# Optimization experiments

Hardware: AMD Instinct MI355X
Metric: run time of the kernel (lower is better)

Reference implementation:

```python
import jax, jax.numpy as jnp
import numpy as np

VOCAB, EMB, HID = 32000, 512, 512
BATCH, SEQ = 32, 512


def setup_inputs() -> dict:
    key = jax.random.key(0)
    ks = jax.random.split(key, 6)
    return {
        "enc_input": jax.random.randint(ks[0], (BATCH, SEQ), 0, VOCAB),
        "emb": jax.random.normal(ks[1], (VOCAB, EMB), dtype=jnp.float32) * 0.02,
        "W_ih": jax.random.normal(ks[2], (2, 3 * HID, EMB), dtype=jnp.float32) * 0.05,
        "W_hh": jax.random.normal(ks[3], (2, 3 * HID, HID), dtype=jnp.float32) * 0.05,
        "b_ih": jax.random.normal(ks[4], (2, 3 * HID), dtype=jnp.float32) * 0.05,
        "b_hh": jax.random.normal(ks[5], (2, 3 * HID), dtype=jnp.float32) * 0.05,
    }


def _gru_dir(gx, W_hh_d, b_hh_d, H):
    # gx: [B, S, 3H] precomputed input gates; scan left-to-right over S.
    B = gx.shape[0]

    def step(h, gxt):
        gh = h @ W_hh_d.T + b_hh_d  # [B, 3H]
        r = jax.nn.sigmoid(gxt[:, :H] + gh[:, :H])
        z = jax.nn.sigmoid(gxt[:, H:2 * H] + gh[:, H:2 * H])
        n = jnp.tanh(gxt[:, 2 * H:] + r * gh[:, 2 * H:])
        h_new = (1.0 - z) * n + z * h
        return h_new, h_new

    h0 = jnp.zeros((B, H), dtype=gx.dtype)
    hT, ys = jax.lax.scan(step, h0, jnp.swapaxes(gx, 0, 1))  # ys: [S, B, H]
    return jnp.swapaxes(ys, 0, 1), hT


def reference(enc_input, emb, W_ih, W_hh, b_ih, b_hh):
    # NOTE: original torch code feeds the bidirectional GRU one timestep at a
    # time, so BOTH directions effectively run left-to-right over the sequence
    # (each with its own weights). We reproduce that exact behavior.
    H = W_hh.shape[-1]
    x = emb[enc_input]  # [B, S, E]
    # Precompute input-gate projections for both directions in one einsum.
    gx = jnp.einsum('bse,dge->bsdg', x, W_ih) + b_ih  # [B, S, 2, 3H]
    out0, h0 = _gru_dir(gx[:, :, 0, :], W_hh[0], b_hh[0], H)
    out1, h1 = _gru_dir(gx[:, :, 1, :], W_hh[1], b_hh[1], H)
    encoded = jnp.concatenate([out0, out1], axis=-1)  # [B, S, 2H]
    hidden = jnp.stack([h0, h1], axis=0)  # [2, B, H]
    return encoded, hidden
```

## Files before the change

kernel.cpp:

```cpp
#include <hip/hip_runtime.h>
#include <stdint.h>

#define VOCAB 32000
#define EMBD 512
#define HID 512
#define BATCH 32
#define SEQL 512

typedef short bf16x8 __attribute__((ext_vector_type(8)));
typedef short bf16x4 __attribute__((ext_vector_type(4)));
typedef float f32x4 __attribute__((ext_vector_type(4)));

static __device__ __forceinline__ float bf2f(short u) {
  union { unsigned u; float f; } c;
  c.u = ((unsigned)(unsigned short)u) << 16;
  return c.f;
}
static __device__ __forceinline__ unsigned short f2bf(float f) {
  union { float f; unsigned u; } c;
  c.f = f;
  unsigned x = c.u;
  unsigned r = (x + 0x7fffu + ((x >> 16) & 1u)) >> 16;
  return (unsigned short)r;
}

__global__ __launch_bounds__(256) void cvt_f32_bf16(
    const float* __restrict__ src, unsigned short* __restrict__ dst, int n8) {
  int i = blockIdx.x * 256 + threadIdx.x;
  if (i >= n8) return;
  const float4* s = (const float4*)src + (size_t)i * 2;
  float4 a = s[0], b = s[1];
  uint4 p;
  p.x = (unsigned)f2bf(a.x) | ((unsigned)f2bf(a.y) << 16);
  p.y = (unsigned)f2bf(a.z) | ((unsigned)f2bf(a.w) << 16);
  p.z = (unsigned)f2bf(b.x) | ((unsigned)f2bf(b.y) << 16);
  p.w = (unsigned)f2bf(b.z) | ((unsigned)f2bf(b.w) << 16);
  ((uint4*)dst)[i] = p;
}

#define GBM 128
#define GBN 128
#define GBK 64

__global__ __launch_bounds__(256) void gemm_gx(
    const int* __restrict__ enc,
    const unsigned short* __restrict__ embb,
    const unsigned short* __restrict__ wih,
    const float* __restrict__ b_ih,
    unsigned short* __restrict__ gx)
{
  __shared__ __align__(16) unsigned short As[GBM * GBK];
  __shared__ __align__(16) unsigned short Bs[GBN * GBK];
  __shared__ int tokl[GBM];

  const int n0 = blockIdx.x * GBN;
  const int m0 = blockIdx.y * GBM;
  const int tid = threadIdx.x;
  if (tid < GBM) {
    int m = m0 + tid;
    tokl[tid] = enc[(m & 31) * SEQL + (m >> 5)];
  }
  __syncthreads();

  const int l = tid & 63, w = tid >> 6;
  const int wr = w >> 1, wc = w & 1;

  f32x4 acc[4][4];
  f32x4 zero = {0.f, 0.f, 0.f, 0.f};
#pragma unroll
  for (int mt = 0; mt < 4; ++mt)
#pragma unroll
    for (int nt = 0; nt < 4; ++nt) acc[mt][nt] = zero;

  for (int kt = 0; kt < 512; kt += GBK) {
#pragma unroll
    for (int it = 0; it < 4; ++it) {
      int c = it * 256 + tid;
      int r = c >> 3, kc = c & 7;
      uint4 v = *(const uint4*)(embb + (size_t)tokl[r] * 512 + kt + kc * 8);
      unsigned off = (unsigned)(r * 128 + kc * 16); off ^= (r & 7) << 4;
      *(uint4*)((char*)As + off) = v;
    }
#pragma unroll
    for (int it = 0; it < 4; ++it) {
      int c = it * 256 + tid;
      int r = c >> 3, kc = c & 7;
      uint4 v = *(const uint4*)(wih + (size_t)(n0 + r) * 512 + kt + kc * 8);
      unsigned off = (unsigned)(r * 128 + kc * 16); off ^= (r & 7) << 4;
      *(uint4*)((char*)Bs + off) = v;
    }
    __syncthreads();
#pragma unroll
    for (int ks = 0; ks < 2; ++ks) {
      bf16x8 af[4], bfr[4];
#pragma unroll
      for (int mt = 0; mt < 4; ++mt) {
        int r = wr * 64 + mt * 16 + (l & 15);
        unsigned off = (unsigned)(r * 128 + ks * 64 + (l >> 4) * 16);
        off ^= (r & 7) << 4;
        af[mt] = *(const bf16x8*)((char*)As + off);
      }
#pragma unroll
      for (int nt = 0; nt < 4; ++nt) {
        int r = wc * 64 + nt * 16 + (l & 15);
        unsigned off = (unsigned)(r * 128 + ks * 64 + (l >> 4) * 16);
        off ^= (r & 7) << 4;
        bfr[nt] = *(const bf16x8*)((char*)Bs + off);
      }
#pragma unroll
      for (int mt = 0; mt < 4; ++mt)
#pragma unroll
        for (int nt = 0; nt < 4; ++nt)
          acc[mt][nt] = __builtin_amdgcn_mfma_f32_16x16x32_bf16(
              af[mt], bfr[nt], acc[mt][nt], 0, 0, 0);
    }
    __syncthreads();
  }

#pragma unroll
  for (int nt = 0; nt < 4; ++nt) {
    int n = n0 + wc * 64 + nt * 16 + (l & 15);
    int d = n >= 1536 ? 1 : 0;
    int g = n - d * 1536;
    float bias = b_ih[n];
#pragma unroll
    for (int mt = 0; mt < 4; ++mt) {
      int mbase = m0 + wr * 64 + mt * 16 + (l >> 4) * 4;
      int s = mbase >> 5;
      int b = mbase & 31;
      unsigned v0 = (unsigned)f2bf(acc[mt][nt][0] + bias) |
                    ((unsigned)f2bf(acc[mt][nt][1] + bias) << 16);
      unsigned v1 = (unsigned)f2bf(acc[mt][nt][2] + bias) |
                    ((unsigned)f2bf(acc[mt][nt][3] + bias) << 16);
      size_t off = ((size_t)(s * 2 + d) * 1536 + g) * 32 + b;
      uint2 pv; pv.x = v0; pv.y = v1;
      *(uint2*)(gx + off) = pv;
    }
  }
}

#define JW 16
#define NWGD 32

__global__ __launch_bounds__(128) void scan_gru(
    const unsigned short* __restrict__ gx,
    const unsigned short* __restrict__ whh,
    const float* __restrict__ bhh,
    unsigned short* __restrict__ hbuf,
    float* __restrict__ out,
    unsigned* __restrict__ flags)
{
  __shared__ __align__(16) unsigned short Wl[48 * 512];

  const int bid = blockIdx.x;
  const int d = bid >> 5;
  const int wg = bid & 31;
  const int j0 = wg * JW;
  const int tid = threadIdx.x;
  const int l = tid & 63;
  const int w = tid >> 6;

  for (int it = 0; it < 24; ++it) {
    int c = it * 128 + tid;
    int lr = c >> 6, kc = c & 63;
    int gate = lr >> 4, jj = lr & 15;
    uint4 v = *(const uint4*)(whh +
        (size_t)(d * 1536 + gate * 512 + j0 + jj) * 512 + kc * 8);
    unsigned off = (unsigned)(lr * 1024 + kc * 16); off ^= (lr & 7) << 4;
    *(uint4*)((char*)Wl + off) = v;
  }

  const int jl = l & 15;
  const int jglob = j0 + jl;
  const int b0 = w * 16;
  const int brow = b0 + (l >> 4) * 4;
  const float bh_r = bhh[d * 1536 + jglob];
  const float bh_z = bhh[d * 1536 + 512 + jglob];
  const float bh_n = bhh[d * 1536 + 1024 + jglob];

  float hold[4] = {0.f, 0.f, 0.f, 0.f};
  unsigned* myflag = flags + (size_t)(d * 32 + wg) * 16;
  const unsigned* fbase = flags + (size_t)d * 32 * 16;

  __syncthreads();

  bf16x4 gr, gz, gn;
  {
    size_t gb = (size_t)d * 1536 * 32;
    gr = *(const bf16x4*)(gx + gb + (size_t)jglob * 32 + brow);
    gz = *(const bf16x4*)(gx + gb + (size_t)(512 + jglob) * 32 + brow);
    gn = *(const bf16x4*)(gx + gb + (size_t)(1024 + jglob) * 32 + brow);
  }

  for (int t = 0; t < SEQL; ++t) {
    f32x4 accr = {0.f, 0.f, 0.f, 0.f};
    f32x4 accz = accr, accn = accr;

    if (t > 0) {
      const unsigned long long* hq = (const unsigned long long*)
          (hbuf + (size_t)(d * 2 + ((t - 1) & 1)) * 32 * 512);
      size_t qb = (size_t)(b0 + (l & 15)) * 128 + (l >> 4) * 2;
      union { unsigned long long q[2]; bf16x8 v; } afu[16];
#pragma unroll
      for (int ks = 0; ks < 16; ++ks) {
        afu[ks].q[0] = __hip_atomic_load(hq + qb + ks * 8,
                                         __ATOMIC_RELAXED, __HIP_MEMORY_SCOPE_AGENT);
        afu[ks].q[1] = __hip_atomic_load(hq + qb + ks * 8 + 1,
                                         __ATOMIC_RELAXED, __HIP_MEMORY_SCOPE_AGENT);
      }
#pragma unroll
      for (int ks = 0; ks < 16; ++ks) {
        unsigned kb = (unsigned)(ks * 64 + (l >> 4) * 16);
        unsigned r0 = (unsigned)jl, r1 = (unsigned)(16 + jl), r2 = (unsigned)(32 + jl);
        bf16x8 bR = *(const bf16x8*)((char*)Wl + ((r0 * 1024 + kb) ^ ((r0 & 7) << 4)));
        bf16x8 bZ = *(const bf16x8*)((char*)Wl + ((r1 * 1024 + kb) ^ ((r1 & 7) << 4)));
        bf16x8 bN = *(const bf16x8*)((char*)Wl + ((r2 * 1024 + kb) ^ ((r2 & 7) << 4)));
        accr = __builtin_amdgcn_mfma_f32_16x16x32_bf16(afu[ks].v, bR, accr, 0, 0, 0);
        accz = __builtin_amdgcn_mfma_f32_16x16x32_bf16(afu[ks].v, bZ, accz, 0, 0, 0);
        accn = __builtin_amdgcn_mfma_f32_16x16x32_bf16(afu[ks].v, bN, accn, 0, 0, 0);
      }
    }

    float hv[4];
#pragma unroll
    for (int i = 0; i < 4; ++i) {
      float ghr = accr[i] + bh_r;
      float ghz = accz[i] + bh_z;
      float ghn = accn[i] + bh_n;
      float pr = bf2f(gr[i]) + ghr;
      float pz = bf2f(gz[i]) + ghz;
      float r = 1.f / (1.f + __expf(-pr));
      float z = 1.f / (1.f + __expf(-pz));
      float n = tanhf(bf2f(gn[i]) + r * ghn);
      float h = (1.f - z) * n + z * hold[i];
      hold[i] = h;
      hv[i] = h;
      out[((size_t)(brow + i) * SEQL + t) * 1024 + d * 512 + jglob] = h;
    }
    if (t == SEQL - 1) {
#pragma unroll
      for (int i = 0; i < 4; ++i)
        out[(size_t)BATCH * SEQL * 1024 +
            (size_t)(d * 32 + brow + i) * 512 + jglob] = hold[i];
    }

    if (t < SEQL - 1) {
      unsigned* hn32 = (unsigned*)(hbuf + (size_t)(d * 2 + (t & 1)) * 32 * 512);
      unsigned mybf[4], pare[4];
#pragma unroll
      for (int i = 0; i < 4; ++i) mybf[i] = f2bf(hv[i]);
#pragma unroll
      for (int i = 0; i < 4; ++i) {
        unsigned ot = (unsigned)__shfl_xor((int)mybf[i], 1);
        pare[i] = (jl & 1) ? (ot | (mybf[i] << 16)) : (mybf[i] | (ot << 16));
      }
      int jc2 = (j0 + (jl & ~1)) >> 1;
      int i0 = (jl & 1) ? 2 : 0;
      __hip_atomic_store(hn32 + (size_t)(brow + i0) * 256 + jc2, pare[i0],
                         __ATOMIC_RELAXED, __HIP_MEMORY_SCOPE_AGENT);
      __hip_atomic_store(hn32 + (size_t)(brow + i0 + 1) * 256 + jc2, pare[i0 + 1],
                         __ATOMIC_RELAXED, __HIP_MEMORY_SCOPE_AGENT);

      bf16x4 ngr, ngz, ngn;
      {
        size_t gb = ((size_t)(t + 1) * 2 + d) * 1536 * 32;
        ngr = *(const bf16x4*)(gx + gb + (size_t)jglob * 32 + brow);
        ngz = *(const bf16x4*)(gx + gb + (size_t)(512 + jglob) * 32 + brow);
        ngn = *(const bf16x4*)(gx + gb + (size_t)(1024 + jglob) * 32 + brow);
      }

      __syncthreads();
      if (w == 0) {
        unsigned tgt = (unsigned)(t + 1);
        if (l == 0)
          __hip_atomic_store(myflag, tgt, __ATOMIC_RELAXED, __HIP_MEMORY_SCOPE_AGENT);
        for (;;) {
          unsigned v = tgt;
          if (l < 32)
            v = __hip_atomic_load(fbase + (size_t)l * 16,
                                  __ATOMIC_RELAXED, __HIP_MEMORY_SCOPE_AGENT);
          if (__ballot(v >= tgt) == ~0ull) break;
          __builtin_amdgcn_s_sleep(1);
        }
      }
      __syncthreads();
      gr = ngr; gz = ngz; gn = ngn;
    }
  }
}

extern "C" void kernel_launch(void* const* d_in, const int* in_sizes, int n_in,
                              void* d_out, int out_size, void* d_ws, size_t ws_size,
                              hipStream_t stream) {
  const int* enc = (const int*)d_in[0];
  const float* emb = (const float*)d_in[1];
  const float* wih = (const float*)d_in[2];
  const float* whh = (const float*)d_in[3];
  const float* bih = (const float*)d_in[4];
  const float* bhh = (const float*)d_in[5];
  float* out = (float*)d_out;

  char* ws = (char*)d_ws;
  unsigned* flags = (unsigned*)ws;
  unsigned short* hbuf = (unsigned short*)(ws + 4096);
  unsigned short* whh_b = (unsigned short*)(ws + 4096 + 131072);
  unsigned short* wih_b = (unsigned short*)(ws + 4096 + 131072 + 3145728);
  unsigned short* emb_b = (unsigned short*)(ws + 4096 + 131072 + 2 * 3145728);
  unsigned short* gx = (unsigned short*)(ws + 4096 + 131072 + 2 * 3145728 + 32768000);

  hipMemsetAsync(flags, 0, 4096, stream);
  cvt_f32_bf16<<<768, 256, 0, stream>>>(whh, whh_b, 196608);
  cvt_f32_bf16<<<768, 256, 0, stream>>>(wih, wih_b, 196608);
  cvt_f32_bf16<<<8000, 256, 0, stream>>>(emb, emb_b, 2048000);
  gemm_gx<<<dim3(24, 128), 256, 0, stream>>>(enc, emb_b, wih_b, bih, gx);
  scan_gru<<<64, 128, 0, stream>>>(gx, whh_b, bhh, hbuf, out, flags);
}
```

Measured before the change: 2.102 ms.

## Replace block-wide barrier with per-wave flag sync and early h publish

Splits the cross-workgroup step flags per wave, so each wave signals its own hidden-state slice and waits only on the matching waves in other workgroups, with no __syncthreads in the step loop. The hidden state is now written to the exchange buffer and its flag set before the output stores, and the spin-wait moves to the start of the next step, just before the h loads. This shortens the serial critical path per timestep. In exchange there are twice as many flags to poll, the next step's gx loads are no longer prefetched before the wait, and correctness depends on an explicit vmcnt wait to order the data stores before the flag store.

```diff
diff --git a/kernel.cpp b/kernel.cpp
--- a/kernel.cpp
+++ b/kernel.cpp
@@ -10,6 +10,9 @@
 typedef short bf16x8 __attribute__((ext_vector_type(8)));
 typedef short bf16x4 __attribute__((ext_vector_type(4)));
 typedef float f32x4 __attribute__((ext_vector_type(4)));
+
+#define AGENT __HIP_MEMORY_SCOPE_AGENT
+#define RLX __ATOMIC_RELAXED
 
 static __device__ __forceinline__ float bf2f(short u) {
   union { unsigned u; float f; } c;
@@ -140,15 +143,14 @@
 }
 
 #define JW 16
-#define NWGD 32
 
 __global__ __launch_bounds__(128) void scan_gru(
     const unsigned short* __restrict__ gx,
     const unsigned short* __restrict__ whh,
     const float* __restrict__ bhh,
     unsigned short* __restrict__ hbuf,
-    float* __restrict__ out,
-    unsigned* __restrict__ flags)
+    unsigned* __restrict__ flags,
+    float* __restrict__ out)
 {
   __shared__ __align__(16) unsigned short Wl[48 * 512];
 
@@ -178,9 +180,10 @@
   const float bh_z = bhh[d * 1536 + 512 + jglob];
   const float bh_n = bhh[d * 1536 + 1024 + jglob];
 
+  unsigned* myflag = flags + ((size_t)(d * 2 + w) * 32 + wg) * 16;
+  const unsigned* fbase = flags + (size_t)(d * 2 + w) * 32 * 16;
+
   float hold[4] = {0.f, 0.f, 0.f, 0.f};
-  unsigned* myflag = flags + (size_t)(d * 32 + wg) * 16;
-  const unsigned* fbase = flags + (size_t)d * 32 * 16;
 
   __syncthreads();
 
@@ -197,16 +200,22 @@
     f32x4 accz = accr, accn = accr;
 
     if (t > 0) {
+      const unsigned tagv = (unsigned)t;
+      for (;;) {
+        unsigned fv = tagv;
+        if (l < 32)
+          fv = __hip_atomic_load(fbase + (size_t)l * 16, RLX, AGENT);
+        if (__ballot(fv >= tagv) == ~0ull) break;
+        __builtin_amdgcn_s_sleep(1);
+      }
       const unsigned long long* hq = (const unsigned long long*)
           (hbuf + (size_t)(d * 2 + ((t - 1) & 1)) * 32 * 512);
       size_t qb = (size_t)(b0 + (l & 15)) * 128 + (l >> 4) * 2;
       union { unsigned long long q[2]; bf16x8 v; } afu[16];
 #pragma unroll
       for (int ks = 0; ks < 16; ++ks) {
-        afu[ks].q[0] = __hip_atomic_load(hq + qb + ks * 8,
-                                         __ATOMIC_RELAXED, __HIP_MEMORY_SCOPE_AGENT);
-        afu[ks].q[1] = __hip_atomic_load(hq + qb + ks * 8 + 1,
-                                         __ATOMIC_RELAXED, __HIP_MEMORY_SCOPE_AGENT);
+        afu[ks].q[0] = __hip_atomic_load(hq + qb + ks * 8, RLX, AGENT);
+        afu[ks].q[1] = __hip_atomic_load(hq + qb + ks * 8 + 1, RLX, AGENT);
       }
 #pragma unroll
       for (int ks = 0; ks < 16; ++ks) {
@@ -221,7 +230,6 @@
       }
     }
 
-    float hv[4];
 #pragma unroll
     for (int i = 0; i < 4; ++i) {
       float ghr = accr[i] + bh_r;
@@ -232,11 +240,33 @@
       float r = 1.f / (1.f + __expf(-pr));
       float z = 1.f / (1.f + __expf(-pz));
       float n = tanhf(bf2f(gn[i]) + r * ghn);
-      float h = (1.f - z) * n + z * hold[i];
-      hold[i] = h;
-      hv[i] = h;
-      out[((size_t)(brow + i) * SEQL + t) * 1024 + d * 512 + jglob] = h;
-    }
+      hold[i] = (1.f - z) * n + z * hold[i];
+    }
+
+    if (t < SEQL - 1) {
+      unsigned* hn32 = (unsigned*)(hbuf + (size_t)(d * 2 + (t & 1)) * 32 * 512);
+      unsigned mybf[4], pare[4];
+#pragma unroll
+      for (int i = 0; i < 4; ++i) mybf[i] = f2bf(hold[i]);
+#pragma unroll
+      for (int i = 0; i < 4; ++i) {
+        unsigned ot = (unsigned)__shfl_xor((int)mybf[i], 1);
+        pare[i] = (jl & 1) ? (ot | (mybf[i] << 16)) : (mybf[i] | (ot << 16));
+      }
+      int jc2 = (j0 + (jl & ~1)) >> 1;
+      int i0 = (jl & 1) ? 2 : 0;
+      __hip_atomic_store(hn32 + (size_t)(brow + i0) * 256 + jc2, pare[i0],
+                         RLX, AGENT);
+      __hip_atomic_store(hn32 + (size_t)(brow + i0 + 1) * 256 + jc2,
+                         pare[i0 + 1], RLX, AGENT);
+      asm volatile("s_waitcnt vmcnt(0)" ::: "memory");
+      if (l == 0)
+        __hip_atomic_store(myflag, (unsigned)(t + 1), RLX, AGENT);
+    }
+
+#pragma unroll
+    for (int i = 0; i < 4; ++i)
+      out[((size_t)(brow + i) * SEQL + t) * 1024 + d * 512 + jglob] = hold[i];
     if (t == SEQL - 1) {
 #pragma unroll
       for (int i = 0; i < 4; ++i)
@@ -245,46 +275,10 @@
     }
 
     if (t < SEQL - 1) {
-      unsigned* hn32 = (unsigned*)(hbuf + (size_t)(d * 2 + (t & 1)) * 32 * 512);
-      unsigned mybf[4], pare[4];
-#pragma unroll
-      for (int i = 0; i < 4; ++i) mybf[i] = f2bf(hv[i]);
-#pragma unroll
-      for (int i = 0; i < 4; ++i) {
-        unsigned ot = (unsigned)__shfl_xor((int)mybf[i], 1);
-        pare[i] = (jl & 1) ? (ot | (mybf[i] << 16)) : (mybf[i] | (ot << 16));
-      }
-      int jc2 = (j0 + (jl & ~1)) >> 1;
-      int i0 = (jl & 1) ? 2 : 0;
-      __hip_atomic_store(hn32 + (size_t)(brow + i0) * 256 + jc2, pare[i0],
-                         __ATOMIC_RELAXED, __HIP_MEMORY_SCOPE_AGENT);
-      __hip_atomic_store(hn32 + (size_t)(brow + i0 + 1) * 256 + jc2, pare[i0 + 1],
-                         __ATOMIC_RELAXED, __HIP_MEMORY_SCOPE_AGENT);
-
-      bf16x4 ngr, ngz, ngn;
-      {
-        size_t gb = ((size_t)(t + 1) * 2 + d) * 1536 * 32;
-        ngr = *(const bf16x4*)(gx + gb + (size_t)jglob * 32 + brow);
-        ngz = *(const bf16x4*)(gx + gb + (size_t)(512 + jglob) * 32 + brow);
-        ngn = *(const bf16x4*)(gx + gb + (size_t)(1024 + jglob) * 32 + brow);
-      }
-
-      __syncthreads();
-      if (w == 0) {
-        unsigned tgt = (unsigned)(t + 1);
-        if (l == 0)
-          __hip_atomic_store(myflag, tgt, __ATOMIC_RELAXED, __HIP_MEMORY_SCOPE_AGENT);
-        for (;;) {
-          unsigned v = tgt;
-          if (l < 32)
-            v = __hip_atomic_load(fbase + (size_t)l * 16,
-                                  __ATOMIC_RELAXED, __HIP_MEMORY_SCOPE_AGENT);
-          if (__ballot(v >= tgt) == ~0ull) break;
-          __builtin_amdgcn_s_sleep(1);
-        }
-      }
-      __syncthreads();
-      gr = ngr; gz = ngz; gn = ngn;
+      size_t gb = ((size_t)(t + 1) * 2 + d) * 1536 * 32;
+      gr = *(const bf16x4*)(gx + gb + (size_t)jglob * 32 + brow);
+      gz = *(const bf16x4*)(gx + gb + (size_t)(512 + jglob) * 32 + brow);
+      gn = *(const bf16x4*)(gx + gb + (size_t)(1024 + jglob) * 32 + brow);
     }
   }
 }
@@ -302,16 +296,16 @@
 
   char* ws = (char*)d_ws;
   unsigned* flags = (unsigned*)ws;
-  unsigned short* hbuf = (unsigned short*)(ws + 4096);
-  unsigned short* whh_b = (unsigned short*)(ws + 4096 + 131072);
-  unsigned short* wih_b = (unsigned short*)(ws + 4096 + 131072 + 3145728);
-  unsigned short* emb_b = (unsigned short*)(ws + 4096 + 131072 + 2 * 3145728);
-  unsigned short* gx = (unsigned short*)(ws + 4096 + 131072 + 2 * 3145728 + 32768000);
-
-  hipMemsetAsync(flags, 0, 4096, stream);
+  unsigned short* hbuf = (unsigned short*)(ws + 8192);
+  unsigned short* whh_b = (unsigned short*)(ws + 139264);
+  unsigned short* wih_b = (unsigned short*)(ws + 139264 + 3145728);
+  unsigned short* emb_b = (unsigned short*)(ws + 139264 + 2 * 3145728);
+  unsigned short* gx = (unsigned short*)(ws + 139264 + 2 * 3145728 + 32768000);
+
+  hipMemsetAsync(flags, 0, 8192, stream);
   cvt_f32_bf16<<<768, 256, 0, stream>>>(whh, whh_b, 196608);
   cvt_f32_bf16<<<768, 256, 0, stream>>>(wih, wih_b, 196608);
   cvt_f32_bf16<<<8000, 256, 0, stream>>>(emb, emb_b, 2048000);
   gemm_gx<<<dim3(24, 128), 256, 0, stream>>>(enc, emb_b, wih_b, bih, gx);
-  scan_gru<<<64, 128, 0, stream>>>(gx, whh_b, bhh, hbuf, out, flags);
-}
+  scan_gru<<<64, 128, 0, stream>>>(gx, whh_b, bhh, hbuf, flags, out);
+}
```

Result: faster. 1.991 ms (median of 2 runs) (-5.3%).
